# Kernel optimization log

Hardware: AMD Instinct MI355X
Metric: run time of the kernel (lower is better)

The kernel has to match this reference:

```python
import jax, jax.numpy as jnp
import numpy as np
import math

D = 1024
L = 4096
B = 4

def setup_inputs() -> dict:
    key = jax.random.key(0)
    ks = jax.random.split(key, 6)
    x = jax.random.normal(ks[0], (B, L, D), dtype=jnp.float32)
    base_phases = jax.random.normal(ks[1], (L, D), dtype=jnp.float32) * math.pi
    s = 1.0 / math.sqrt(D)
    W_v = jax.random.normal(ks[2], (D, D), dtype=jnp.float32) * s
    b_v = jnp.zeros((D,), dtype=jnp.float32)
    ln_g = jnp.ones((D,), dtype=jnp.float32)
    ln_b = jnp.zeros((D,), dtype=jnp.float32)
    W_o = jax.random.normal(ks[3], (D, D), dtype=jnp.float32) * s
    b_o = jnp.zeros((D,), dtype=jnp.float32)
    return {"x": x, "base_phases": base_phases, "W_v": W_v, "b_v": b_v,
            "ln_g": ln_g, "ln_b": ln_b, "W_o": W_o, "b_o": b_o}

def _layernorm(x, g, b, eps=1e-5):
    mu = jnp.mean(x, axis=-1, keepdims=True)
    var = jnp.mean(jnp.square(x - mu), axis=-1, keepdims=True)
    return (x - mu) * jax.lax.rsqrt(var + eps) * g + b

def reference(x, base_phases, W_v, b_v, ln_g, ln_b, W_o, b_o):
    Bv, Lv, Dv = x.shape
    phases = base_phases[:Lv][None, :, :]          # [1, L, D]
    cosp, sinp = jnp.cos(phases), jnp.sin(phases)
    value = jnp.einsum('bld,ed->ble', x, W_v) + b_v  # Linear(D,D)
    mem_real = jnp.cumsum(value * cosp, axis=1)
    mem_imag = jnp.cumsum(value * sinp, axis=1)
    retrieved = (mem_real * cosp + mem_imag * sinp) / math.sqrt(Dv)
    out = jnp.einsum('bld,ed->ble', _layernorm(retrieved, ln_g, ln_b), W_o) + b_o
    return x + out
```

## Files before the change

### kernel.cpp

```cpp
#include <hip/hip_runtime.h>
#include <stdint.h>


#define D_DIM 1024
#define L_DIM 4096
#define B_DIM 4
#define M_DIM (B_DIM * L_DIM)
#define CHUNK 64
#define NCH (L_DIM / CHUNK)
#define NT 16

typedef __attribute__((ext_vector_type(8))) short short8;
typedef __attribute__((ext_vector_type(4))) float f32x4;

__device__ __forceinline__ float bf2f(uint32_t h) {
  union { uint32_t u; float f; } x; x.u = h << 16; return x.f;
}
__device__ __forceinline__ uint16_t f2bf(float f) {
  union { float f; uint32_t u; } x; x.f = f;
  uint32_t u = x.u;
  u += 0x7fffu + ((u >> 16) & 1u);
  return (uint16_t)(u >> 16);
}

__global__ void k_prep(const float* __restrict__ x, const float* __restrict__ Wv,
                       const float* __restrict__ Wo, const float* __restrict__ g,
                       const float* __restrict__ bln, const float* __restrict__ bo,
                       uint16_t* __restrict__ xb, uint16_t* __restrict__ wv,
                       uint16_t* __restrict__ wob, float* __restrict__ u,
                       float* __restrict__ vb) {
  int blk = blockIdx.x;
  int tid = threadIdx.x;
  if (blk < 8192 + 512) {
    const float* in = (blk < 8192) ? x : Wv;
    uint16_t* outp = (blk < 8192) ? xb : wv;
    int base = (blk < 8192) ? blk : (blk - 8192);
    int i = (base * 256 + tid) * 8;
    float4 a = *(const float4*)(in + i);
    float4 b = *(const float4*)(in + i + 4);
    ushort4 o0 = { f2bf(a.x), f2bf(a.y), f2bf(a.z), f2bf(a.w) };
    ushort4 o1 = { f2bf(b.x), f2bf(b.y), f2bf(b.z), f2bf(b.w) };
    *(ushort4*)(outp + i) = o0;
    *(ushort4*)(outp + i + 4) = o1;
    return;
  }
  int e = blk - 8704;
  int d = tid * 4;
  float4 w  = *(const float4*)(Wo + (size_t)e * D_DIM + d);
  float4 gg = *(const float4*)(g + d);
  float4 bb = *(const float4*)(bln + d);
  float gw0 = gg.x * w.x, gw1 = gg.y * w.y, gw2 = gg.z * w.z, gw3 = gg.w * w.w;
  ushort4 o = { f2bf(gw0), f2bf(gw1), f2bf(gw2), f2bf(gw3) };
  *(ushort4*)(wob + (size_t)e * D_DIM + d) = o;
  float su = gw0 + gw1 + gw2 + gw3;
  float sv = bb.x * w.x + bb.y * w.y + bb.z * w.z + bb.w * w.w;
#pragma unroll
  for (int off = 32; off > 0; off >>= 1) {
    su += __shfl_down(su, off);
    sv += __shfl_down(sv, off);
  }
  __shared__ float s1[4], s2[4];
  int wid = tid >> 6, lane = tid & 63;
  if (lane == 0) { s1[wid] = su; s2[wid] = sv; }
  __syncthreads();
  if (tid == 0) {
    u[e]  = s1[0] + s1[1] + s1[2] + s1[3];
    vb[e] = s2[0] + s2[1] + s2[2] + s2[3] + bo[e];
  }
}

template <int MODE>
__global__ __launch_bounds__(512, 2) void k_gemm(
    const uint16_t* __restrict__ A, const uint16_t* __restrict__ W,
    void* __restrict__ outp,
    const float* __restrict__ p0, const float* __restrict__ p1,
    const float* __restrict__ mu, const float* __restrict__ inv,
    const uint16_t* __restrict__ xres) {
  __shared__ char lds[8 * 16384];
  const int tid = threadIdx.x;
  const int lane = tid & 63;
  const int wid = tid >> 6;
  const int wm = wid >> 2;
  const int wn = wid & 3;

  const int idx = blockIdx.x;
  const int bm = (idx & 7) * 8 + ((idx >> 3) >> 2);
  const int bn = (idx >> 3) & 3;

  const int srow = tid >> 3;
  const int scb  = (tid & 7) * 16;
  const int scbs = scb ^ ((srow & 7) << 4);

#define GLL(SRC, DST)                                                            \
  __builtin_amdgcn_global_load_lds((const __attribute__((address_space(1))) void*)(SRC), \
                                   (__attribute__((address_space(3))) void*)(DST), 16, 0, 0)

#define STAGE_A(KS, HA)                                                          \
  do {                                                                           \
    char* _d = lds + ((((KS)&1) * 4 + (HA)) << 14) + tid * 16;                   \
    const char* _s = (const char*)A +                                            \
        (size_t)(bm * 256 + (HA) * 128 + srow) * 2048 + (KS) * 128 + scbs;       \
    GLL(_s, _d);                                                                 \
    GLL(_s + (size_t)64 * 2048, _d + 8192);                                      \
  } while (0)

#define STAGE_B(KS, HB)                                                          \
  do {                                                                           \
    char* _d = lds + ((((KS)&1) * 4 + 2 + (HB)) << 14) + tid * 16;               \
    const char* _s = (const char*)W +                                            \
        (size_t)(bn * 256 + (HB) * 128 + srow) * 2048 + (KS) * 128 + scbs;       \
    GLL(_s, _d);                                                                 \
    GLL(_s + (size_t)64 * 2048, _d + 8192);                                      \
  } while (0)

  const int axor = (lane & 7) << 4;
  const int afr  = lane & 15;
  const int acol = (lane >> 4) * 16;

#define LD_A(PAR, I, KK)                                                         \
  (*(const short8*)(lds + (((PAR) * 4 + wm) << 14) + ((I) * 16 + afr) * 128 +    \
                    (((KK) * 64 + acol) ^ axor)))
#define LD_B(PAR, J, KK)                                                         \
  (*(const short8*)(lds + (((PAR) * 4 + 2 + (wn >> 1)) << 14) +                  \
                    ((wn & 1) * 64 + (J) * 16 + afr) * 128 +                     \
                    (((KK) * 64 + acol) ^ axor)))

#define MFMA(AV, BV, CV) __builtin_amdgcn_mfma_f32_16x16x32_bf16(AV, BV, CV, 0, 0, 0)
#define SB0() __builtin_amdgcn_sched_barrier(0)

  f32x4 acc[8][4];
#pragma unroll
  for (int i = 0; i < 8; ++i)
#pragma unroll
    for (int j = 0; j < 4; ++j)
      acc[i][j] = (f32x4){0.f, 0.f, 0.f, 0.f};

  STAGE_B(0, 0); STAGE_B(0, 1);
  STAGE_A(0, 0); STAGE_A(0, 1);
  asm volatile("s_waitcnt vmcnt(2)" ::: "memory");
  __builtin_amdgcn_s_barrier();

  for (int ks = 0; ks < NT; ++ks) {
    const int par = ks & 1;
    short8 Af0, Af1, Af2, Af3, Bf0, Bf1, Bf2, Bf3;

    Bf0 = LD_B(par, 0, 0); Bf1 = LD_B(par, 1, 0); Bf2 = LD_B(par, 2, 0); Bf3 = LD_B(par, 3, 0);
    Af0 = LD_A(par, 0, 0); Af1 = LD_A(par, 1, 0); Af2 = LD_A(par, 2, 0); Af3 = LD_A(par, 3, 0);
    SB0();
    if (ks + 1 < NT) STAGE_B(ks + 1, 0);
    __builtin_amdgcn_s_barrier();
    asm volatile("s_waitcnt lgkmcnt(0)" ::: "memory");
    SB0();
    __builtin_amdgcn_s_setprio(1);
#pragma unroll
    for (int j = 0; j < 4; ++j) {
      const short8 bj = (j == 0) ? Bf0 : (j == 1) ? Bf1 : (j == 2) ? Bf2 : Bf3;
      acc[0][j] = MFMA(Af0, bj, acc[0][j]);
      acc[1][j] = MFMA(Af1, bj, acc[1][j]);
      acc[2][j] = MFMA(Af2, bj, acc[2][j]);
      acc[3][j] = MFMA(Af3, bj, acc[3][j]);
    }
    __builtin_amdgcn_s_setprio(0);
    if (ks == NT - 1) { asm volatile("s_waitcnt vmcnt(0)" ::: "memory"); }
    else              { asm volatile("s_waitcnt vmcnt(2)" ::: "memory"); }
    __builtin_amdgcn_s_barrier();

    Af0 = LD_A(par, 4, 0); Af1 = LD_A(par, 5, 0); Af2 = LD_A(par, 6, 0); Af3 = LD_A(par, 7, 0);
    SB0();
    if (ks + 1 < NT) STAGE_B(ks + 1, 1);
    __builtin_amdgcn_s_barrier();
    asm volatile("s_waitcnt lgkmcnt(0)" ::: "memory");
    SB0();
    __builtin_amdgcn_s_setprio(1);
#pragma unroll
    for (int j = 0; j < 4; ++j) {
      const short8 bj = (j == 0) ? Bf0 : (j == 1) ? Bf1 : (j == 2) ? Bf2 : Bf3;
      acc[4][j] = MFMA(Af0, bj, acc[4][j]);
      acc[5][j] = MFMA(Af1, bj, acc[5][j]);
      acc[6][j] = MFMA(Af2, bj, acc[6][j]);
      acc[7][j] = MFMA(Af3, bj, acc[7][j]);
    }
    __builtin_amdgcn_s_setprio(0);
    __builtin_amdgcn_s_barrier();

    Bf0 = LD_B(par, 0, 1); Bf1 = LD_B(par, 1, 1); Bf2 = LD_B(par, 2, 1); Bf3 = LD_B(par, 3, 1);
    Af0 = LD_A(par, 0, 1); Af1 = LD_A(par, 1, 1); Af2 = LD_A(par, 2, 1); Af3 = LD_A(par, 3, 1);
    SB0();
    if (ks + 1 < NT) STAGE_A(ks + 1, 0);
    __builtin_amdgcn_s_barrier();
    asm volatile("s_waitcnt lgkmcnt(0)" ::: "memory");
    SB0();
    __builtin_amdgcn_s_setprio(1);
#pragma unroll
    for (int j = 0; j < 4; ++j) {
      const short8 bj = (j == 0) ? Bf0 : (j == 1) ? Bf1 : (j == 2) ? Bf2 : Bf3;
      acc[0][j] = MFMA(Af0, bj, acc[0][j]);
      acc[1][j] = MFMA(Af1, bj, acc[1][j]);
      acc[2][j] = MFMA(Af2, bj, acc[2][j]);
      acc[3][j] = MFMA(Af3, bj, acc[3][j]);
    }
    __builtin_amdgcn_s_setprio(0);
    __builtin_amdgcn_s_barrier();

    Af0 = LD_A(par, 4, 1); Af1 = LD_A(par, 5, 1); Af2 = LD_A(par, 6, 1); Af3 = LD_A(par, 7, 1);
    SB0();
    if (ks + 1 < NT) STAGE_A(ks + 1, 1);
    __builtin_amdgcn_s_barrier();
    asm volatile("s_waitcnt lgkmcnt(0)" ::: "memory");
    SB0();
    __builtin_amdgcn_s_setprio(1);
#pragma unroll
    for (int j = 0; j < 4; ++j) {
      const short8 bj = (j == 0) ? Bf0 : (j == 1) ? Bf1 : (j == 2) ? Bf2 : Bf3;
      acc[4][j] = MFMA(Af0, bj, acc[4][j]);
      acc[5][j] = MFMA(Af1, bj, acc[5][j]);
      acc[6][j] = MFMA(Af2, bj, acc[6][j]);
      acc[7][j] = MFMA(Af3, bj, acc[7][j]);
    }
    __builtin_amdgcn_s_setprio(0);
    if (ks < NT - 1) { asm volatile("s_waitcnt vmcnt(2)" ::: "memory"); }
    __builtin_amdgcn_s_barrier();
  }

  if (MODE == 0) {
    uint16_t* outv = (uint16_t*)outp;
    __syncthreads();
#pragma unroll
    for (int i = 0; i < 8; ++i)
#pragma unroll
      for (int r = 0; r < 4; ++r) {
        int row = wm * 128 + i * 16 + (lane >> 4) * 4 + r;
#pragma unroll
        for (int j = 0; j < 4; ++j) {
          int ncol = wn * 64 + j * 16 + (lane & 15);
          float v = acc[i][j][r] + p0[bn * 256 + ncol];
          *(uint16_t*)(lds + row * 512 + ((ncol * 2) ^ ((row & 7) << 4))) = f2bf(v);
        }
      }
    __syncthreads();
    {
      int row = tid >> 1, half = tid & 1;
      uint16_t* gdst = outv + (size_t)(bm * 256 + row) * D_DIM + bn * 256 + half * 128;
#pragma unroll
      for (int s = 0; s < 16; ++s) {
        short8 v = *(const short8*)(lds + row * 512 +
                                    ((half * 256 + s * 16) ^ ((row & 7) << 4)));
        *(short8*)(gdst + s * 8) = v;
      }
    }
  } else {
    float* outf = (float*)outp;
#pragma unroll
    for (int i = 0; i < 8; ++i)
#pragma unroll
      for (int r = 0; r < 4; ++r) {
        int m = bm * 256 + wm * 128 + i * 16 + (lane >> 4) * 4 + r;
        float im = inv[m], mm = mu[m];
#pragma unroll
        for (int j = 0; j < 4; ++j) {
          int n = bn * 256 + wn * 64 + j * 16 + (lane & 15);
          outf[(size_t)m * D_DIM + n] =
              im * acc[i][j][r] - im * mm * p0[n] + p1[n] +
              bf2f(xres[(size_t)m * D_DIM + n]);
        }
      }
  }
#undef GLL
#undef STAGE_A
#undef STAGE_B
#undef LD_A
#undef LD_B
#undef MFMA
#undef SB0
}

__global__ void k_passA(const uint16_t* __restrict__ value, const float* __restrict__ phases,
                        float* __restrict__ pr, float* __restrict__ pi) {
  int d0 = blockIdx.x * 512 + threadIdx.x * 2;
  int c = blockIdx.y, b = blockIdx.z;
  const uint16_t* vp = value + ((size_t)(b * L_DIM + c * CHUNK)) * D_DIM + d0;
  const float* pp = phases + (size_t)(c * CHUNK) * D_DIM + d0;
  float sr0 = 0, si0 = 0, sr1 = 0, si1 = 0;
#pragma unroll 4
  for (int l = 0; l < CHUNK; ++l) {
    uint32_t vv = *(const uint32_t*)vp; vp += D_DIM;
    float2 ph = *(const float2*)pp; pp += D_DIM;
    float v0 = bf2f(vv & 0xffffu), v1 = bf2f(vv >> 16);
    float s0, c0, s1, c1;
    __sincosf(ph.x, &s0, &c0);
    __sincosf(ph.y, &s1, &c1);
    sr0 += v0 * c0; si0 += v0 * s0;
    sr1 += v1 * c1; si1 += v1 * s1;
  }
  size_t o = ((size_t)b * NCH + c) * D_DIM + d0;
  *(float2*)(pr + o) = make_float2(sr0, sr1);
  *(float2*)(pi + o) = make_float2(si0, si1);
}

__global__ void k_passB(float* __restrict__ pr, float* __restrict__ pi) {
  int d = blockIdx.x * 256 + threadIdx.x;
  int b = blockIdx.y;
  size_t base = (size_t)b * NCH * D_DIM + d;
  float r[NCH], im[NCH];
#pragma unroll
  for (int c = 0; c < NCH; ++c) r[c] = pr[base + (size_t)c * D_DIM];
#pragma unroll
  for (int c = 0; c < NCH; ++c) im[c] = pi[base + (size_t)c * D_DIM];
  float rr = 0, ri = 0;
#pragma unroll
  for (int c = 0; c < NCH; ++c) {
    float t = r[c]; r[c] = rr; rr += t;
    t = im[c]; im[c] = ri; ri += t;
  }
#pragma unroll
  for (int c = 0; c < NCH; ++c) pr[base + (size_t)c * D_DIM] = r[c];
#pragma unroll
  for (int c = 0; c < NCH; ++c) pi[base + (size_t)c * D_DIM] = im[c];
}

__global__ void k_passC(const uint16_t* __restrict__ value, const float* __restrict__ phases,
                        const float* __restrict__ pr, const float* __restrict__ pi,
                        uint16_t* __restrict__ ret) {
  int d0 = blockIdx.x * 512 + threadIdx.x * 2;
  int c = blockIdx.y, b = blockIdx.z;
  size_t o = ((size_t)b * NCH + c) * D_DIM + d0;
  float2 r0 = *(const float2*)(pr + o);
  float2 i0 = *(const float2*)(pi + o);
  float mr0 = r0.x, mr1 = r0.y, mi0 = i0.x, mi1 = i0.y;
  size_t rowoff = ((size_t)(b * L_DIM + c * CHUNK)) * D_DIM + d0;
  const uint16_t* vp = value + rowoff;
  uint16_t* rp = ret + rowoff;
  const float* pp = phases + (size_t)(c * CHUNK) * D_DIM + d0;
  const float isd = 0.03125f;
#pragma unroll 4
  for (int l = 0; l < CHUNK; ++l) {
    uint32_t vv = *(const uint32_t*)vp; vp += D_DIM;
    float2 ph = *(const float2*)pp; pp += D_DIM;
    float v0 = bf2f(vv & 0xffffu), v1 = bf2f(vv >> 16);
    float s0, c0, s1, c1;
    __sincosf(ph.x, &s0, &c0);
    __sincosf(ph.y, &s1, &c1);
    mr0 += v0 * c0; mi0 += v0 * s0;
    mr1 += v1 * c1; mi1 += v1 * s1;
    float o0 = (mr0 * c0 + mi0 * s0) * isd;
    float o1 = (mr1 * c1 + mi1 * s1) * isd;
    *(uint32_t*)rp = (uint32_t)f2bf(o0) | ((uint32_t)f2bf(o1) << 16);
    rp += D_DIM;
  }
}

__global__ void k_stats(const uint16_t* __restrict__ ret, float* __restrict__ mu,
                        float* __restrict__ inv) {
  int m = blockIdx.x, tid = threadIdx.x;
  ushort4 v = *(const ushort4*)(ret + (size_t)m * D_DIM + tid * 4);
  float f0 = bf2f(v.x), f1 = bf2f(v.y), f2_ = bf2f(v.z), f3 = bf2f(v.w);
  float s = f0 + f1 + f2_ + f3;
  float ss = f0 * f0 + f1 * f1 + f2_ * f2_ + f3 * f3;
#pragma unroll
  for (int off = 32; off > 0; off >>= 1) {
    s += __shfl_down(s, off);
    ss += __shfl_down(ss, off);
  }
  __shared__ float a1[4], a2[4];
  int wid = tid >> 6, lane = tid & 63;
  if (lane == 0) { a1[wid] = s; a2[wid] = ss; }
  __syncthreads();
  if (tid == 0) {
    float S = a1[0] + a1[1] + a1[2] + a1[3];
    float SS = a2[0] + a2[1] + a2[2] + a2[3];
    float mm = S * (1.0f / 1024.0f);
    float var = SS * (1.0f / 1024.0f) - mm * mm;
    mu[m] = mm;
    inv[m] = rsqrtf(var + 1e-5f);
  }
}

extern "C" void kernel_launch(void* const* d_in, const int* in_sizes, int n_in,
                              void* d_out, int out_size, void* d_ws, size_t ws_size,
                              hipStream_t stream) {
  const float* x      = (const float*)d_in[0];
  const float* phases = (const float*)d_in[1];
  const float* Wv     = (const float*)d_in[2];
  const float* bv     = (const float*)d_in[3];
  const float* lng    = (const float*)d_in[4];
  const float* lnb    = (const float*)d_in[5];
  const float* Wo     = (const float*)d_in[6];
  const float* bo     = (const float*)d_in[7];
  float* out = (float*)d_out;

  char* ws = (char*)d_ws;
  uint16_t* xb    = (uint16_t*)(ws);
  uint16_t* value = (uint16_t*)(ws + (32ull << 20));
  uint16_t* wv    = (uint16_t*)(ws + (64ull << 20));
  uint16_t* wob   = (uint16_t*)(ws + (66ull << 20));
  float* pr       = (float*)(ws + (68ull << 20));
  float* pi       = (float*)(ws + (69ull << 20));
  float* u        = (float*)(ws + (70ull << 20));
  float* vb       = (float*)(ws + (70ull << 20) + 4096);
  float* mu       = (float*)(ws + (71ull << 20));
  float* inv      = (float*)(ws + (72ull << 20));
  uint16_t* retr  = value;

  k_prep<<<8192 + 512 + 1024, 256, 0, stream>>>(x, Wv, Wo, lng, lnb, bo,
                                                xb, wv, wob, u, vb);
  k_gemm<0><<<(M_DIM / 256) * (D_DIM / 256), 512, 0, stream>>>(
      xb, wv, value, bv, nullptr, nullptr, nullptr, nullptr);
  k_passA<<<dim3(2, NCH, B_DIM), 256, 0, stream>>>(value, phases, pr, pi);
  k_passB<<<dim3(D_DIM / 256, B_DIM), 256, 0, stream>>>(pr, pi);
  k_passC<<<dim3(2, NCH, B_DIM), 256, 0, stream>>>(value, phases, pr, pi, retr);
  k_stats<<<M_DIM, 256, 0, stream>>>(retr, mu, inv);
  k_gemm<1><<<(M_DIM / 256) * (D_DIM / 256), 512, 0, stream>>>(
      retr, wob, out, u, vb, mu, inv, xb);
}
```

Measured before the change: 148.7 us.

## Fuse chunk phase-sum into value GEMM epilogue and LayerNorm stats into scan pass

The per-chunk cos/sin-weighted sums (former passA) are now computed in the first GEMM's epilogue from the bf16 value tile already held in LDS, so the separate value re-read kernel is removed. The row mean and variance partial sums are computed inside passC via wave shuffles and LDS. The two halves are written to a small buffer and combined in the output GEMM's epilogue, which removes the k_stats kernel and its re-read of the retrieved tensor. This cuts two launches and two full passes over the bf16 activations. In exchange the GEMM epilogue gains sincos work and phase loads, and passC gains per-row reductions and loses its unroll pragma.

```diff
diff --git a/kernel.cpp b/kernel.cpp
--- a/kernel.cpp
+++ b/kernel.cpp
@@ -74,7 +74,8 @@
     const uint16_t* __restrict__ A, const uint16_t* __restrict__ W,
     void* __restrict__ outp,
     const float* __restrict__ p0, const float* __restrict__ p1,
-    const float* __restrict__ mu, const float* __restrict__ inv,
+    const float* __restrict__ phases, float* __restrict__ prp,
+    float* __restrict__ pip, const float2* __restrict__ sbuf,
     const uint16_t* __restrict__ xres) {
   __shared__ char lds[8 * 16384];
   const int tid = threadIdx.x;
@@ -248,14 +249,45 @@
         *(short8*)(gdst + s * 8) = v;
       }
     }
+    {
+      int c = tid >> 7;
+      int g = tid & 127;
+      int lrow0 = c * 64;
+      int lphase = (bm & 15) * 256 + lrow0;
+      int bidx = bm >> 4;
+      int dcol = bn * 256 + g * 2;
+      const float* pp = phases + (size_t)lphase * D_DIM + dcol;
+      float sr0 = 0, si0 = 0, sr1 = 0, si1 = 0;
+#pragma unroll 4
+      for (int rr = 0; rr < 64; ++rr) {
+        int row = lrow0 + rr;
+        int sw = (row & 7) << 4;
+        float v0 = bf2f(*(const uint16_t*)(lds + row * 512 + ((g * 4) ^ sw)));
+        float v1 = bf2f(*(const uint16_t*)(lds + row * 512 + ((g * 4 + 2) ^ sw)));
+        float2 ph = *(const float2*)pp; pp += D_DIM;
+        float s0, c0, s1, c1;
+        __sincosf(ph.x, &s0, &c0);
+        __sincosf(ph.y, &s1, &c1);
+        sr0 += v0 * c0; si0 += v0 * s0;
+        sr1 += v1 * c1; si1 += v1 * s1;
+      }
+      size_t o = ((size_t)bidx * NCH + ((bm & 15) * 4 + c)) * D_DIM + dcol;
+      *(float2*)(prp + o) = make_float2(sr0, sr1);
+      *(float2*)(pip + o) = make_float2(si0, si1);
+    }
   } else {
     float* outf = (float*)outp;
+    const float2* sb0 = sbuf;
+    const float2* sb1 = sbuf + M_DIM;
 #pragma unroll
     for (int i = 0; i < 8; ++i)
 #pragma unroll
       for (int r = 0; r < 4; ++r) {
         int m = bm * 256 + wm * 128 + i * 16 + (lane >> 4) * 4 + r;
-        float im = inv[m], mm = mu[m];
+        float2 a0 = sb0[m], a1 = sb1[m];
+        float s = a0.x + a1.x, ss = a0.y + a1.y;
+        float mm = s * (1.0f / 1024.0f);
+        float im = rsqrtf(ss * (1.0f / 1024.0f) - mm * mm + 1e-5f);
 #pragma unroll
         for (int j = 0; j < 4; ++j) {
           int n = bn * 256 + wn * 64 + j * 16 + (lane & 15);
@@ -274,29 +306,6 @@
 #undef SB0
 }
 
-__global__ void k_passA(const uint16_t* __restrict__ value, const float* __restrict__ phases,
-                        float* __restrict__ pr, float* __restrict__ pi) {
-  int d0 = blockIdx.x * 512 + threadIdx.x * 2;
-  int c = blockIdx.y, b = blockIdx.z;
-  const uint16_t* vp = value + ((size_t)(b * L_DIM + c * CHUNK)) * D_DIM + d0;
-  const float* pp = phases + (size_t)(c * CHUNK) * D_DIM + d0;
-  float sr0 = 0, si0 = 0, sr1 = 0, si1 = 0;
-#pragma unroll 4
-  for (int l = 0; l < CHUNK; ++l) {
-    uint32_t vv = *(const uint32_t*)vp; vp += D_DIM;
-    float2 ph = *(const float2*)pp; pp += D_DIM;
-    float v0 = bf2f(vv & 0xffffu), v1 = bf2f(vv >> 16);
-    float s0, c0, s1, c1;
-    __sincosf(ph.x, &s0, &c0);
-    __sincosf(ph.y, &s1, &c1);
-    sr0 += v0 * c0; si0 += v0 * s0;
-    sr1 += v1 * c1; si1 += v1 * s1;
-  }
-  size_t o = ((size_t)b * NCH + c) * D_DIM + d0;
-  *(float2*)(pr + o) = make_float2(sr0, sr1);
-  *(float2*)(pi + o) = make_float2(si0, si1);
-}
-
 __global__ void k_passB(float* __restrict__ pr, float* __restrict__ pi) {
   int d = blockIdx.x * 256 + threadIdx.x;
   int b = blockIdx.y;
@@ -320,9 +329,12 @@
 
 __global__ void k_passC(const uint16_t* __restrict__ value, const float* __restrict__ phases,
                         const float* __restrict__ pr, const float* __restrict__ pi,
-                        uint16_t* __restrict__ ret) {
-  int d0 = blockIdx.x * 512 + threadIdx.x * 2;
+                        uint16_t* __restrict__ ret, float2* __restrict__ sbuf) {
+  __shared__ float lds_s[CHUNK][4], lds_ss[CHUNK][4];
+  int tid = threadIdx.x;
+  int d0 = blockIdx.x * 512 + tid * 2;
   int c = blockIdx.y, b = blockIdx.z;
+  int w = tid >> 6, lane = tid & 63;
   size_t o = ((size_t)b * NCH + c) * D_DIM + d0;
   float2 r0 = *(const float2*)(pr + o);
   float2 i0 = *(const float2*)(pi + o);
@@ -332,7 +344,6 @@
   uint16_t* rp = ret + rowoff;
   const float* pp = phases + (size_t)(c * CHUNK) * D_DIM + d0;
   const float isd = 0.03125f;
-#pragma unroll 4
   for (int l = 0; l < CHUNK; ++l) {
     uint32_t vv = *(const uint32_t*)vp; vp += D_DIM;
     float2 ph = *(const float2*)pp; pp += D_DIM;
@@ -344,34 +355,25 @@
     mr1 += v1 * c1; mi1 += v1 * s1;
     float o0 = (mr0 * c0 + mi0 * s0) * isd;
     float o1 = (mr1 * c1 + mi1 * s1) * isd;
-    *(uint32_t*)rp = (uint32_t)f2bf(o0) | ((uint32_t)f2bf(o1) << 16);
+    uint32_t pk = (uint32_t)f2bf(o0) | ((uint32_t)f2bf(o1) << 16);
+    *(uint32_t*)rp = pk;
     rp += D_DIM;
-  }
-}
-
-__global__ void k_stats(const uint16_t* __restrict__ ret, float* __restrict__ mu,
-                        float* __restrict__ inv) {
-  int m = blockIdx.x, tid = threadIdx.x;
-  ushort4 v = *(const ushort4*)(ret + (size_t)m * D_DIM + tid * 4);
-  float f0 = bf2f(v.x), f1 = bf2f(v.y), f2_ = bf2f(v.z), f3 = bf2f(v.w);
-  float s = f0 + f1 + f2_ + f3;
-  float ss = f0 * f0 + f1 * f1 + f2_ * f2_ + f3 * f3;
-#pragma unroll
-  for (int off = 32; off > 0; off >>= 1) {
-    s += __shfl_down(s, off);
-    ss += __shfl_down(ss, off);
-  }
-  __shared__ float a1[4], a2[4];
-  int wid = tid >> 6, lane = tid & 63;
-  if (lane == 0) { a1[wid] = s; a2[wid] = ss; }
+    float q0 = bf2f(pk & 0xffffu), q1 = bf2f(pk >> 16);
+    float sr = q0 + q1;
+    float sq = q0 * q0 + q1 * q1;
+#pragma unroll
+    for (int off = 32; off > 0; off >>= 1) {
+      sr += __shfl_down(sr, off);
+      sq += __shfl_down(sq, off);
+    }
+    if (lane == 0) { lds_s[l][w] = sr; lds_ss[l][w] = sq; }
+  }
   __syncthreads();
-  if (tid == 0) {
-    float S = a1[0] + a1[1] + a1[2] + a1[3];
-    float SS = a2[0] + a2[1] + a2[2] + a2[3];
-    float mm = S * (1.0f / 1024.0f);
-    float var = SS * (1.0f / 1024.0f) - mm * mm;
-    mu[m] = mm;
-    inv[m] = rsqrtf(var + 1e-5f);
+  if (tid < CHUNK) {
+    float s = lds_s[tid][0] + lds_s[tid][1] + lds_s[tid][2] + lds_s[tid][3];
+    float ss = lds_ss[tid][0] + lds_ss[tid][1] + lds_ss[tid][2] + lds_ss[tid][3];
+    int m = b * L_DIM + c * CHUNK + tid;
+    sbuf[(size_t)blockIdx.x * M_DIM + m] = make_float2(s, ss);
   }
 }
 
@@ -397,18 +399,15 @@
   float* pi       = (float*)(ws + (69ull << 20));
   float* u        = (float*)(ws + (70ull << 20));
   float* vb       = (float*)(ws + (70ull << 20) + 4096);
-  float* mu       = (float*)(ws + (71ull << 20));
-  float* inv      = (float*)(ws + (72ull << 20));
+  float2* sbuf    = (float2*)(ws + (71ull << 20));
   uint16_t* retr  = value;
 
   k_prep<<<8192 + 512 + 1024, 256, 0, stream>>>(x, Wv, Wo, lng, lnb, bo,
                                                 xb, wv, wob, u, vb);
   k_gemm<0><<<(M_DIM / 256) * (D_DIM / 256), 512, 0, stream>>>(
-      xb, wv, value, bv, nullptr, nullptr, nullptr, nullptr);
-  k_passA<<<dim3(2, NCH, B_DIM), 256, 0, stream>>>(value, phases, pr, pi);
+      xb, wv, value, bv, nullptr, phases, pr, pi, nullptr, nullptr);
   k_passB<<<dim3(D_DIM / 256, B_DIM), 256, 0, stream>>>(pr, pi);
-  k_passC<<<dim3(2, NCH, B_DIM), 256, 0, stream>>>(value, phases, pr, pi, retr);
-  k_stats<<<M_DIM, 256, 0, stream>>>(retr, mu, inv);
+  k_passC<<<dim3(2, NCH, B_DIM), 256, 0, stream>>>(value, phases, pr, pi, retr, sbuf);
   k_gemm<1><<<(M_DIM / 256) * (D_DIM / 256), 512, 0, stream>>>(
-      retr, wob, out, u, vb, mu, inv, xb);
-}
+      retr, wob, out, u, vb, nullptr, nullptr, nullptr, sbuf, xb);
+}
```

Result: slower. 164.2 us (+10.4%).
